# Kernel optimization log

Hardware: AMD Instinct MI355X
Metric: run time of the kernel (lower is better)

Reference implementation:

```python
import jax, jax.numpy as jnp
import numpy as np

B, T, V, C = 64, 256, 256, 4
NEG = -jnp.inf


def setup_inputs() -> dict:
    key = jax.random.key(0)
    k1, k2, k3 = jax.random.split(key, 3)
    logits = jax.random.normal(k1, (B, T, V, C), dtype=jnp.float32)
    ar_sent = jax.random.randint(k2, (B, T), 0, 61, dtype=jnp.int32)
    en_sent = jax.random.randint(k3, (B, V), 0, 61, dtype=jnp.int32)
    return {"logits": logits, "ar_sent": ar_sent, "en_sent": en_sent}


def _forward_alpha(ins, dele, sub):
    # ins/dele/sub: [B,T,V] log-scores of insertion/deletion/substitution into cell (t,v)
    b, t_len, v_len = ins.shape
    z = jnp.zeros((b, 1), ins.dtype)
    # row t=0: only insertions -> prefix sum
    alpha0 = jnp.concatenate([z, jnp.cumsum(ins[:, 0, 1:], axis=1)], axis=1)

    def step(prev, xs):
        ins_t, del_t, sub_t = xs  # each [B,V]
        # c[v]: contributions from previous row (deletion + substitution)
        c = jnp.concatenate(
            [del_t[:, :1] + prev[:, :1],
             jnp.logaddexp(del_t[:, 1:] + prev[:, 1:], sub_t[:, 1:] + prev[:, :-1])],
            axis=1)
        # within-row recurrence alpha[v] = logaddexp(ins[v]+alpha[v-1], c[v])
        # solved in closed form: alpha[v] = S[v] + logcumsumexp_k<=v (c[k]-S[k]), S=prefix sum of ins
        s = jnp.concatenate([z, jnp.cumsum(ins_t[:, 1:], axis=1)], axis=1)
        row = s + jax.lax.cumlogsumexp(c - s, axis=1)
        return row, row

    xs = (jnp.moveaxis(ins, 1, 0)[1:], jnp.moveaxis(dele, 1, 0)[1:], jnp.moveaxis(sub, 1, 0)[1:])
    _, rows = jax.lax.scan(step, alpha0, xs)
    return jnp.moveaxis(jnp.concatenate([alpha0[None], rows], axis=0), 0, 1)  # [B,T,V]


def _backward_beta(ins, dele, sub):
    b, t_len, v_len = ins.shape
    z = jnp.zeros((b, 1), ins.dtype)
    # row t=T-1: only insertions -> suffix sum, corner = 0
    ins_last = ins[:, -1, :]
    beta_last = jnp.concatenate([jnp.cumsum(ins_last[:, -2::-1], axis=1)[:, ::-1], z], axis=1)

    def step(nxt, xs):
        ins_t, del_t, sub_t = xs
        # c[v]: contributions from next row (deletion + substitution); v=V-1 has no substitution
        c = jnp.concatenate(
            [jnp.logaddexp(del_t[:, :-1] + nxt[:, :-1], sub_t[:, :-1] + nxt[:, 1:]),
             del_t[:, -1:] + nxt[:, -1:]],
            axis=1)
        # beta[v] = logaddexp(ins[v]+beta[v+1], c[v]): reverse linear recurrence -> flip + closed form
        fins = ins_t[:, ::-1]
        fc = c[:, ::-1]
        fs = jnp.concatenate([z, jnp.cumsum(fins[:, 1:], axis=1)], axis=1)
        fb = fs + jax.lax.cumlogsumexp(fc - fs, axis=1)
        row = fb[:, ::-1]
        return row, row

    xs = (jnp.moveaxis(ins, 1, 0)[:-1][::-1],
          jnp.moveaxis(dele, 1, 0)[:-1][::-1],
          jnp.moveaxis(sub, 1, 0)[:-1][::-1])
    _, rows = jax.lax.scan(step, beta_last, xs)
    beta = jnp.concatenate([rows[::-1], beta_last[None]], axis=0)
    return jnp.moveaxis(beta, 0, 1)  # [B,T,V]


def reference(logits, ar_sent, en_sent):
    # tiny_table class ids: deletion=0, insertion=1, substitution=2 (constant, char-independent)
    scores = jax.nn.log_softmax(logits, axis=3)  # [B,T,V,4]
    dele, ins, sub = scores[..., 0], scores[..., 1], scores[..., 2]
    alpha = _forward_alpha(ins, dele, sub)

    # beta / expected counts are computed under no_grad in the original
    sg = jax.lax.stop_gradient
    s = sg(scores)
    a = sg(alpha)
    beta = _backward_beta(s[..., 1], s[..., 0], s[..., 2])

    bsz, t_len, v_len, n_cls = scores.shape
    cls = jnp.arange(n_cls)[None, None, :]
    t_lt = (jnp.arange(t_len) < t_len - 1)[:, None, None]
    v_lt = (jnp.arange(v_len) < v_len - 1)[None, :, None]
    pd = jnp.broadcast_to(jnp.where((cls == 0) & t_lt, 0.0, NEG), (t_len, v_len, n_cls))
    pi = jnp.broadcast_to(jnp.where((cls == 1) & v_lt, 0.0, NEG), (t_len, v_len, n_cls))
    ps = jnp.broadcast_to(jnp.where((cls == 2) & t_lt & v_lt, 0.0, NEG), (t_len, v_len, n_cls))

    full = jnp.full((bsz, t_len, v_len, n_cls), NEG, scores.dtype)
    ed = full.at[:, 1:].set(a[:, :-1, :, None] + s[:, 1:] + pd[None, 1:] + beta[:, 1:, :, None])
    ei = full.at[:, :, 1:].set(a[:, :, :-1, None] + s[:, :, 1:] + pi[None, :, 1:] + beta[:, :, 1:, None])
    es = full.at[:, 1:, 1:].set(
        a[:, :-1, :-1, None] + s[:, 1:, 1:] + ps[None, 1:, 1:] + beta[:, 1:, 1:, None])

    ec = jnp.logaddexp(jnp.logaddexp(ed, ei), es)
    norm = jax.nn.logsumexp(ec, axis=3, keepdims=True)
    norm = jnp.where(jnp.isneginf(norm), 0.0, norm)  # avoid nan at degenerate (0,0)-type cells
    expected_counts = jnp.exp(ec - norm)
    return (scores, expected_counts, alpha[0, -1, -1])
```

## Files before the change

kernel.cpp:

```cpp
#include <hip/hip_runtime.h>
#include <math.h>

#define BB 64
#define TT 256
#define VV 256
#define SLABS 321
#define SLAB_F (SLABS * 256)
#define PLANE ((size_t)BB * SLAB_F)
#define EPLANE ((size_t)BB * SLABS * 64)
#define NSLAB_W 319

typedef __attribute__((ext_vector_type(4))) _Float16 half4;

__device__ __forceinline__ float dpp_shr1_f(float x) {
    return __int_as_float(__builtin_amdgcn_update_dpp(
        __float_as_int(x), __float_as_int(x), 0x138, 0xF, 0xF, false));
}
__device__ __forceinline__ int dpp_shr1_i(int x) {
    return __builtin_amdgcn_update_dpp(x, x, 0x138, 0xF, 0xF, false);
}

__device__ __forceinline__ float lae2(float x, float y) {
    float m = fmaxf(x, y);
    float d = x - y;
    return m + __logf(1.0f + __expf(-fabsf(d)));
}

__global__ void __launch_bounds__(256) k_prep(const float4* __restrict__ lg,
                                              float4* __restrict__ sc,
                                              _Float16* __restrict__ Dd,
                                              _Float16* __restrict__ Di,
                                              _Float16* __restrict__ Du) {
    int blk = blockIdx.x;
    int b = blk / NSLAB_W;
    int s = blk - b * NSLAB_W;
    int v = threadIdx.x;
    int t = s - (v >> 2);
    bool valid = (t >= 0) && (t < TT);
    int tc = valid ? t : 0;
    size_t ci = ((size_t)b << 16) | ((size_t)tc << 8) | (size_t)v;
    float4 x = lg[ci];
    float m = fmaxf(fmaxf(x.x, x.y), fmaxf(x.z, x.w));
    float e0 = __expf(x.x - m), e1 = __expf(x.y - m);
    float e2 = __expf(x.z - m), e3 = __expf(x.w - m);
    float ssum = e0 + e1 + e2 + e3;
    float l = m + __logf(ssum);
    if (valid) sc[ci] = make_float4(x.x - l, x.y - l, x.z - l, x.w - l);
    float rcp = valid ? (1.0f / ssum) : 0.0f;
    size_t pb = (size_t)b * SLAB_F + ((size_t)s << 8) + v;
    Dd[pb] = (_Float16)(e0 * rcp);
    Di[pb] = (_Float16)(e1 * rcp);
    Du[pb] = (_Float16)(e2 * rcp);
}

__global__ void __launch_bounds__(128) k_dp(const _Float16* __restrict__ Pd,
                                            const _Float16* __restrict__ Pi,
                                            const _Float16* __restrict__ Pu,
                                            float* __restrict__ A,
                                            int* __restrict__ Ei,
                                            float* __restrict__ scalar_out) {
    const int b = (blockIdx.x << 1) | (threadIdx.x >> 6);
    const int lane = threadIdx.x & 63;
    const bool l0 = (lane == 0);
    const size_t base = (size_t)b * SLAB_F + (lane << 2);

    const half4* __restrict__ pd = (const half4*)(Pd + base);
    const half4* __restrict__ pi = (const half4*)(Pi + base);
    const half4* __restrict__ pu = (const half4*)(Pu + base);
    float4* __restrict__ pa = (float4*)(A + base);
    int* __restrict__ pe = Ei + (size_t)b * SLABS * 64 + lane;
    const int SS = 64;

    half4 d0,d1,d2,d3,d4,d5,d6,d7;
    half4 i0,i1,i2,i3,i4,i5,i6,i7;
    half4 u0,u1,u2,u3,u4,u5,u6,u7;
    d0 = pd[0*SS]; i0 = pi[0*SS]; u0 = pu[0*SS];
    d1 = pd[1*SS]; i1 = pi[1*SS]; u1 = pu[1*SS];
    d2 = pd[2*SS]; i2 = pi[2*SS]; u2 = pu[2*SS];
    d3 = pd[3*SS]; i3 = pi[3*SS]; u3 = pu[3*SS];
    d4 = pd[4*SS]; i4 = pi[4*SS]; u4 = pu[4*SS];
    d5 = pd[5*SS]; i5 = pi[5*SS]; u5 = pu[5*SS];
    d6 = pd[6*SS]; i6 = pi[6*SS]; u6 = pu[6*SS];
    d7 = pd[7*SS]; i7 = pi[7*SS]; u7 = pu[7*SS];

    float A0 = 0.0f, A1 = 0.0f, A2 = 0.0f, A3 = 0.0f;
    int   E  = 0;
    float LC = 0.0f, LP = 0.0f;
    int   EC = 0,    EP = 0;
    float sA3 = 0.0f;
    int   sEn = 0;

    int s = 0;

#define STEP(DD, II, UU, FIXUP, CLAMP, CAP)                                       \
    {                                                                             \
        const half4 dl = DD, in = II, su = UU;                                    \
        {                                                                         \
            int sp = s + 8;                                                       \
            if (CLAMP) sp = sp > SLABS - 1 ? SLABS - 1 : sp;                      \
            DD = pd[sp * SS]; II = pi[sp * SS]; UU = pu[sp * SS];                 \
        }                                                                         \
        int E_eff = E;                                                            \
        bool isT0 = false;                                                        \
        if (FIXUP) {                                                              \
            isT0 = (s == lane);                                                   \
            E_eff = isT0 ? (l0 ? 0 : EC) : E;                                     \
        }                                                                         \
        const float lc = l0 ? 0.0f : ldexpf(LC, EC - E_eff);                      \
        const float lp = l0 ? 0.0f : ldexpf(LP, EP - E_eff);                      \
        float X0 = (float)dl.x * A0 + (float)su.x * lp;                           \
        float X1 = (float)dl.y * A1 + (float)su.y * A0;                           \
        float X2 = (float)dl.z * A2 + (float)su.z * A1;                           \
        float X3 = (float)dl.w * A3 + (float)su.w * A2;                           \
        if (FIXUP && isT0) {                                                      \
            X0 = l0 ? 1.0f : 0.0f; X1 = 0.0f; X2 = 0.0f; X3 = 0.0f;               \
        }                                                                         \
        const float iy = (float)in.y, iz = (float)in.z, iw = (float)in.w;         \
        const float B0 = X0;                                                      \
        const float B1 = fmaf(B0, iy, X1);                                        \
        const float B2 = fmaf(B1, iz, X2);                                        \
        const float B3 = fmaf(B2, iw, X3);                                        \
        const float Q0 = (float)in.x;                                             \
        const float Q1 = Q0 * iy;                                                 \
        const float Q2 = Q1 * iz;                                                 \
        const float Q3 = Q2 * iw;                                                 \
        float nA0 = fmaf(lc, Q0, B0);                                             \
        float nA1 = fmaf(lc, Q1, B1);                                             \
        float nA2 = fmaf(lc, Q2, B2);                                             \
        float nA3 = fmaf(lc, Q3, B3);                                             \
        const int eb = (int)((__float_as_uint(nA3) >> 23) & 255u) - 126;          \
        const int En = E_eff + eb;                                                \
        nA3 = ldexpf(nA3, -eb);                                                   \
        nA0 = ldexpf(nA0, -eb);                                                   \
        nA1 = ldexpf(nA1, -eb);                                                   \
        nA2 = ldexpf(nA2, -eb);                                                   \
        LP = LC; EP = EC;                                                         \
        LC = dpp_shr1_f(nA3);                                                     \
        EC = dpp_shr1_i(En);                                                      \
        pa[s * SS] = make_float4(nA0, nA1, nA2, nA3);                             \
        pe[s * 64] = En;                                                          \
        if (CAP && s == TT + 62) { sA3 = nA3; sEn = En; }     \
        A0 = nA0; A1 = nA1; A2 = nA2; A3 = nA3; E = En;                           \
        ++s;                                                                      \
    }

#pragma unroll 1
    for (int it = 0; it < 8; ++it) {
        STEP(d0, i0, u0, 1, 0, 0);
        STEP(d1, i1, u1, 1, 0, 0);
        STEP(d2, i2, u2, 1, 0, 0);
        STEP(d3, i3, u3, 1, 0, 0);
        STEP(d4, i4, u4, 1, 0, 0);
        STEP(d5, i5, u5, 1, 0, 0);
        STEP(d6, i6, u6, 1, 0, 0);
        STEP(d7, i7, u7, 1, 0, 0);
    }
#pragma unroll 1
    for (int it = 0; it < 31; ++it) {
        STEP(d0, i0, u0, 0, 0, 0);
        STEP(d1, i1, u1, 0, 0, 0);
        STEP(d2, i2, u2, 0, 0, 0);
        STEP(d3, i3, u3, 0, 0, 0);
        STEP(d4, i4, u4, 0, 0, 0);
        STEP(d5, i5, u5, 0, 0, 0);
        STEP(d6, i6, u6, 0, 0, 0);
        STEP(d7, i7, u7, 0, 0, 0);
    }
    STEP(d0, i0, u0, 0, 1, 1);
    STEP(d1, i1, u1, 0, 1, 1);
    STEP(d2, i2, u2, 0, 1, 1);
    STEP(d3, i3, u3, 0, 1, 1);
    STEP(d4, i4, u4, 0, 1, 1);
    STEP(d5, i5, u5, 0, 1, 1);
    STEP(d6, i6, u6, 0, 1, 1);
    STEP(d7, i7, u7, 0, 1, 1);
#undef STEP

    if ((b == 0) && (lane == 63))
        scalar_out[0] = logf(sA3) + (float)sEn * 0.6931471805599453f;
}

__global__ void __launch_bounds__(256) k_counts(const _Float16* __restrict__ Pd,
                                                const _Float16* __restrict__ Pi,
                                                const _Float16* __restrict__ Pu,
                                                const float* __restrict__ A,
                                                const int* __restrict__ Ei,
                                                float4* __restrict__ out) {
    int blk = blockIdx.x;
    int b = blk / NSLAB_W;
    int s = blk - b * NSLAB_W;
    int v = threadIdx.x;
    int g = v >> 2;
    int t = s - g;
    if ((t < 0) | (t >= TT)) return;

    size_t ab = (size_t)b * SLAB_F;
    size_t ebp = (size_t)b * SLABS * 64;
    int sm1 = s > 0 ? s - 1 : 0;
    int sm2 = s > 1 ? s - 2 : 0;
    int vm = v ? v - 1 : 0;
    int gm = g ? g - 1 : 0;
    bool v4 = (v & 3) == 0;

    float pD = (float)Pd[ab + ((size_t)s << 8) + v];
    float pI = (float)Pi[ab + ((size_t)s << 8) + v];
    float pU = (float)Pu[ab + ((size_t)s << 8) + v];
    float AA = A[ab + ((size_t)s   << 8) + v];
    float AU = A[ab + ((size_t)sm1 << 8) + v];
    int   EA = Ei[ebp + s   * 64 + g];
    int   EU = Ei[ebp + sm1 * 64 + g];
    float AL = v4 ? A[ab + ((size_t)sm1 << 8) + vm] : A[ab + ((size_t)s   << 8) + vm];
    int   EL = v4 ? Ei[ebp + sm1 * 64 + gm] : EA;
    float AD = v4 ? A[ab + ((size_t)sm2 << 8) + vm] : A[ab + ((size_t)sm1 << 8) + vm];
    int   ED = v4 ? Ei[ebp + sm2 * 64 + gm] : EU;

    bool tE = (t == 0) | (t == TT - 1);
    bool vE = (v == 0) | (v == VV - 1);
    float inv = 1.0f / AA;
    float w0 = ldexpf(pD * AU * inv, EU - EA);
    float w1 = ldexpf(pI * AL * inv, EL - EA);
    float w2 = ldexpf(pU * AD * inv, ED - EA);
    float4 o;
    o.x = tE ? 0.0f : (vE ? 1.0f : w0);
    o.y = vE ? 0.0f : (tE ? 1.0f : w1);
    o.z = (tE | vE) ? 0.0f : w2;
    o.w = 0.0f;
    out[((size_t)b << 16) | ((size_t)t << 8) | (size_t)v] = o;
}

__global__ void k_prep_legacy(const float4* __restrict__ lg, float4* __restrict__ sc, int n) {
    int i = blockIdx.x * blockDim.x + threadIdx.x;
    int st = gridDim.x * blockDim.x;
    for (; i < n; i += st) {
        float4 x = lg[i];
        float m = fmaxf(fmaxf(x.x, x.y), fmaxf(x.z, x.w));
        float s = __expf(x.x - m) + __expf(x.y - m) + __expf(x.z - m) + __expf(x.w - m);
        float l = m + __logf(s);
        sc[i] = make_float4(x.x - l, x.y - l, x.z - l, x.w - l);
    }
}
__global__ void __launch_bounds__(64) k_dp_legacy(const float4* __restrict__ scores,
                                                  float4* __restrict__ counts,
                                                  float* __restrict__ scalar_out) {
    const int b = blockIdx.x;
    const int lane = threadIdx.x;
    const int v0 = lane << 2;
    const float4* __restrict__ srow = scores + ((size_t)b * TT * VV + v0);
    float4* __restrict__ crow = counts + ((size_t)b * TT * VV + v0);
    float4 P0[4], P1[4], P2[4];
    {
        int r; const float4* p;
        r = 0 - lane; r = r < 0 ? 0 : r; p = srow + (size_t)r * VV;
        P0[0]=p[0]; P0[1]=p[1]; P0[2]=p[2]; P0[3]=p[3];
        r = 1 - lane; r = r < 0 ? 0 : r; p = srow + (size_t)r * VV;
        P1[0]=p[0]; P1[1]=p[1]; P1[2]=p[2]; P1[3]=p[3];
        r = 2 - lane; r = r < 0 ? 0 : r; p = srow + (size_t)r * VV;
        P2[0]=p[0]; P2[1]=p[1]; P2[2]=p[2]; P2[3]=p[3];
    }
    float aPrev[4] = { -INFINITY, -INFINITY, -INFINITY, -INFINITY };
    float leftPrev = -INFINITY, leftCur = -INFINITY;
    int s = 0;
#define STEPL(BUF)                                                                \
    {                                                                             \
        const int t = s - lane;                                                   \
        const bool active = (t >= 0) && (t < TT);                                 \
        float4 c0 = BUF[0], c1 = BUF[1], c2 = BUF[2], c3 = BUF[3];                \
        {                                                                         \
            int tp = t + 3; tp = tp < 0 ? 0 : tp; tp = tp > TT - 1 ? TT - 1 : tp; \
            const float4* lp = srow + (size_t)tp * VV;                            \
            BUF[0]=lp[0]; BUF[1]=lp[1]; BUF[2]=lp[2]; BUF[3]=lp[3];               \
        }                                                                         \
        float aPm1_0 = (lane == 0) ? -INFINITY : leftPrev;                        \
        float cv0 = lae2(c0.x + aPrev[0], c0.z + aPm1_0);                         \
        float cv1 = lae2(c1.x + aPrev[1], c1.z + aPrev[0]);                       \
        float cv2 = lae2(c2.x + aPrev[2], c2.z + aPrev[1]);                       \
        float cv3 = lae2(c3.x + aPrev[3], c3.z + aPrev[2]);                       \
        if (lane == 0) cv0 = c0.x + aPrev[0];                                     \
        if (t == 0) {                                                             \
            cv0 = (lane == 0) ? 0.0f : -INFINITY;                                 \
            cv1 = -INFINITY; cv2 = -INFINITY; cv3 = -INFINITY;                    \
        }                                                                         \
        float lc = (lane == 0) ? -INFINITY : leftCur;                             \
        float a0 = lae2(lc + c0.y, cv0);                                          \
        float a1 = lae2(a0 + c1.y, cv1);                                          \
        float a2 = lae2(a1 + c2.y, cv2);                                          \
        float a3 = lae2(a2 + c3.y, cv3);                                          \
        if (active) {                                                             \
            const bool tE = (t == 0) | (t == TT - 1);                             \
            float aCm1[4] = { lc, a0, a1, a2 };                                   \
            float aPm1[4] = { aPm1_0, aPrev[0], aPrev[1], aPrev[2] };             \
            float aP[4]   = { aPrev[0], aPrev[1], aPrev[2], aPrev[3] };           \
            float aA[4]   = { a0, a1, a2, a3 };                                   \
            float4 sv[4]  = { c0, c1, c2, c3 };                                   \
            float4* cp = crow + (size_t)t * VV;                                   \
            _Pragma("unroll")                                                     \
            for (int k = 0; k < 4; ++k) {                                         \
                const bool vE = (k == 0 && lane == 0) || (k == 3 && lane == 63);  \
                float w0 = __expf(aP[k]   + sv[k].x - aA[k]);                     \
                float w1 = __expf(aCm1[k] + sv[k].y - aA[k]);                     \
                float w2 = __expf(aPm1[k] + sv[k].z - aA[k]);                     \
                float4 o;                                                         \
                o.x = tE ? 0.0f : (vE ? 1.0f : w0);                               \
                o.y = vE ? 0.0f : (tE ? 1.0f : w1);                               \
                o.z = (tE || vE) ? 0.0f : w2;                                     \
                o.w = 0.0f;                                                       \
                cp[k] = o;                                                        \
            }                                                                     \
            if ((t == TT - 1) && (lane == 63) && (b == 0)) scalar_out[0] = a3;    \
        }                                                                         \
        aPrev[0]=a0; aPrev[1]=a1; aPrev[2]=a2; aPrev[3]=a3;                       \
        leftPrev = leftCur;                                                       \
        leftCur = __shfl_up(a3, 1);                                               \
        ++s;                                                                      \
    }
#pragma unroll 1
    for (int it = 0; it < 107; ++it) { STEPL(P0); STEPL(P1); STEPL(P2); }
#undef STEPL
}

extern "C" void kernel_launch(void* const* d_in, const int* in_sizes, int n_in,
                              void* d_out, int out_size, void* d_ws, size_t ws_size,
                              hipStream_t stream) {
    const float* logits = (const float*)d_in[0];
    float* out = (float*)d_out;
    const size_t ncell = (size_t)BB * TT * VV;

    float4* scores = (float4*)out;
    float4* counts = (float4*)(out + ncell * 4);
    float* scalar_out = out + ncell * 8;

    _Float16* Pd = (_Float16*)d_ws;
    _Float16* Pi = Pd + PLANE;
    _Float16* Pu = Pi + PLANE;
    float* Aa = (float*)(Pu + PLANE);
    int*   Ee = (int*)(Aa + PLANE);

    size_t need = PLANE * 2 * 3 + PLANE * 4 + EPLANE * 4;
    if (ws_size >= need) {
        k_prep<<<BB * NSLAB_W, 256, 0, stream>>>((const float4*)logits, scores, Pd, Pi, Pu);
        k_dp<<<BB / 2, 128, 0, stream>>>(Pd, Pi, Pu, Aa, Ee, scalar_out);
        k_counts<<<BB * NSLAB_W, 256, 0, stream>>>(Pd, Pi, Pu, Aa, Ee, counts);
    } else {
        k_prep_legacy<<<2048, 256, 0, stream>>>((const float4*)logits, scores, (int)ncell);
        k_dp_legacy<<<BB, 64, 0, stream>>>(scores, counts, scalar_out);
    }
}
```

Before: 112.4 us.

## Fuse DP scan and counts into one kernel with progress-flag overlap

Merges the serial DP kernel and the counts kernel into a single launch. 32 blocks run the wavefront recurrence and publish per-batch progress through release atomics every 32 slabs. The remaining persistent blocks spin on those flags and compute expected counts for completed slabs, so the counts pass overlaps the latency-bound DP instead of running after it. This adds a memset, spin-wait polling and fences, and it relies on the DP blocks being scheduled alongside the consumer blocks to avoid deadlock.

```diff
diff --git a/kernel.cpp b/kernel.cpp
--- a/kernel.cpp
+++ b/kernel.cpp
@@ -9,6 +9,7 @@
 #define PLANE ((size_t)BB * SLAB_F)
 #define EPLANE ((size_t)BB * SLABS * 64)
 #define NSLAB_W 319
+#define NCNT 704
 
 typedef __attribute__((ext_vector_type(4))) _Float16 half4;
 
@@ -53,44 +54,47 @@
     Du[pb] = (_Float16)(e2 * rcp);
 }
 
-__global__ void __launch_bounds__(128) k_dp(const _Float16* __restrict__ Pd,
-                                            const _Float16* __restrict__ Pi,
-                                            const _Float16* __restrict__ Pu,
-                                            float* __restrict__ A,
-                                            int* __restrict__ Ei,
-                                            float* __restrict__ scalar_out) {
-    const int b = (blockIdx.x << 1) | (threadIdx.x >> 6);
-    const int lane = threadIdx.x & 63;
-    const bool l0 = (lane == 0);
-    const size_t base = (size_t)b * SLAB_F + (lane << 2);
-
-    const half4* __restrict__ pd = (const half4*)(Pd + base);
-    const half4* __restrict__ pi = (const half4*)(Pi + base);
-    const half4* __restrict__ pu = (const half4*)(Pu + base);
-    float4* __restrict__ pa = (float4*)(A + base);
-    int* __restrict__ pe = Ei + (size_t)b * SLABS * 64 + lane;
-    const int SS = 64;
-
-    half4 d0,d1,d2,d3,d4,d5,d6,d7;
-    half4 i0,i1,i2,i3,i4,i5,i6,i7;
-    half4 u0,u1,u2,u3,u4,u5,u6,u7;
-    d0 = pd[0*SS]; i0 = pi[0*SS]; u0 = pu[0*SS];
-    d1 = pd[1*SS]; i1 = pi[1*SS]; u1 = pu[1*SS];
-    d2 = pd[2*SS]; i2 = pi[2*SS]; u2 = pu[2*SS];
-    d3 = pd[3*SS]; i3 = pi[3*SS]; u3 = pu[3*SS];
-    d4 = pd[4*SS]; i4 = pi[4*SS]; u4 = pu[4*SS];
-    d5 = pd[5*SS]; i5 = pi[5*SS]; u5 = pu[5*SS];
-    d6 = pd[6*SS]; i6 = pi[6*SS]; u6 = pu[6*SS];
-    d7 = pd[7*SS]; i7 = pi[7*SS]; u7 = pu[7*SS];
-
-    float A0 = 0.0f, A1 = 0.0f, A2 = 0.0f, A3 = 0.0f;
-    int   E  = 0;
-    float LC = 0.0f, LP = 0.0f;
-    int   EC = 0,    EP = 0;
-    float sA3 = 0.0f;
-    int   sEn = 0;
-
-    int s = 0;
+__global__ void __launch_bounds__(256) k_dpcnt(const _Float16* __restrict__ Pd,
+                                               const _Float16* __restrict__ Pi,
+                                               const _Float16* __restrict__ Pu,
+                                               float* __restrict__ A,
+                                               int* __restrict__ Ei,
+                                               float* __restrict__ scalar_out,
+                                               int* __restrict__ progress,
+                                               float4* __restrict__ out) {
+    if (blockIdx.x < 32) {
+        if (threadIdx.x >= 128) return;
+        const int b = (blockIdx.x << 1) | (threadIdx.x >> 6);
+        const int lane = threadIdx.x & 63;
+        const bool l0 = (lane == 0);
+        const size_t base = (size_t)b * SLAB_F + (lane << 2);
+
+        const half4* __restrict__ pd = (const half4*)(Pd + base);
+        const half4* __restrict__ pi = (const half4*)(Pi + base);
+        const half4* __restrict__ pu = (const half4*)(Pu + base);
+        float4* __restrict__ pa = (float4*)(A + base);
+        int* __restrict__ pe = Ei + (size_t)b * SLABS * 64 + lane;
+        const int SS = 64;
+
+        half4 d0,d1,d2,d3,d4,d5,d6,d7;
+        half4 i0,i1,i2,i3,i4,i5,i6,i7;
+        half4 u0,u1,u2,u3,u4,u5,u6,u7;
+        d0 = pd[0*SS]; i0 = pi[0*SS]; u0 = pu[0*SS];
+        d1 = pd[1*SS]; i1 = pi[1*SS]; u1 = pu[1*SS];
+        d2 = pd[2*SS]; i2 = pi[2*SS]; u2 = pu[2*SS];
+        d3 = pd[3*SS]; i3 = pi[3*SS]; u3 = pu[3*SS];
+        d4 = pd[4*SS]; i4 = pi[4*SS]; u4 = pu[4*SS];
+        d5 = pd[5*SS]; i5 = pi[5*SS]; u5 = pu[5*SS];
+        d6 = pd[6*SS]; i6 = pi[6*SS]; u6 = pu[6*SS];
+        d7 = pd[7*SS]; i7 = pi[7*SS]; u7 = pu[7*SS];
+
+        float A0 = 0.0f, A1 = 0.0f, A2 = 0.0f, A3 = 0.0f;
+        int   E  = 0;
+        float LC = 0.0f, LP = 0.0f;
+        int   EC = 0,    EP = 0;
+        float sA3 = 0.0f;
+        int   sEn = 0;
+        int s = 0;
 
 #define STEP(DD, II, UU, FIXUP, CLAMP, CAP)                                       \
     {                                                                             \
@@ -139,93 +143,112 @@
         EC = dpp_shr1_i(En);                                                      \
         pa[s * SS] = make_float4(nA0, nA1, nA2, nA3);                             \
         pe[s * 64] = En;                                                          \
-        if (CAP && s == TT + 62) { sA3 = nA3; sEn = En; }     \
+        if (CAP && s == TT + 62) { sA3 = nA3; sEn = En; }                         \
         A0 = nA0; A1 = nA1; A2 = nA2; A3 = nA3; E = En;                           \
         ++s;                                                                      \
     }
+#define PUBLISH()                                                                 \
+    {                                                                             \
+        __threadfence();                                                          \
+        if (l0) __hip_atomic_store(&progress[b], s - 1, __ATOMIC_RELEASE,         \
+                                   __HIP_MEMORY_SCOPE_AGENT);                     \
+    }
 
 #pragma unroll 1
-    for (int it = 0; it < 8; ++it) {
-        STEP(d0, i0, u0, 1, 0, 0);
-        STEP(d1, i1, u1, 1, 0, 0);
-        STEP(d2, i2, u2, 1, 0, 0);
-        STEP(d3, i3, u3, 1, 0, 0);
-        STEP(d4, i4, u4, 1, 0, 0);
-        STEP(d5, i5, u5, 1, 0, 0);
-        STEP(d6, i6, u6, 1, 0, 0);
-        STEP(d7, i7, u7, 1, 0, 0);
-    }
+        for (int it = 0; it < 8; ++it) {
+            STEP(d0, i0, u0, 1, 0, 0);
+            STEP(d1, i1, u1, 1, 0, 0);
+            STEP(d2, i2, u2, 1, 0, 0);
+            STEP(d3, i3, u3, 1, 0, 0);
+            STEP(d4, i4, u4, 1, 0, 0);
+            STEP(d5, i5, u5, 1, 0, 0);
+            STEP(d6, i6, u6, 1, 0, 0);
+            STEP(d7, i7, u7, 1, 0, 0);
+            if ((it & 3) == 3) PUBLISH();
+        }
 #pragma unroll 1
-    for (int it = 0; it < 31; ++it) {
-        STEP(d0, i0, u0, 0, 0, 0);
-        STEP(d1, i1, u1, 0, 0, 0);
-        STEP(d2, i2, u2, 0, 0, 0);
-        STEP(d3, i3, u3, 0, 0, 0);
-        STEP(d4, i4, u4, 0, 0, 0);
-        STEP(d5, i5, u5, 0, 0, 0);
-        STEP(d6, i6, u6, 0, 0, 0);
-        STEP(d7, i7, u7, 0, 0, 0);
-    }
-    STEP(d0, i0, u0, 0, 1, 1);
-    STEP(d1, i1, u1, 0, 1, 1);
-    STEP(d2, i2, u2, 0, 1, 1);
-    STEP(d3, i3, u3, 0, 1, 1);
-    STEP(d4, i4, u4, 0, 1, 1);
-    STEP(d5, i5, u5, 0, 1, 1);
-    STEP(d6, i6, u6, 0, 1, 1);
-    STEP(d7, i7, u7, 0, 1, 1);
+        for (int it = 0; it < 31; ++it) {
+            STEP(d0, i0, u0, 0, 0, 0);
+            STEP(d1, i1, u1, 0, 0, 0);
+            STEP(d2, i2, u2, 0, 0, 0);
+            STEP(d3, i3, u3, 0, 0, 0);
+            STEP(d4, i4, u4, 0, 0, 0);
+            STEP(d5, i5, u5, 0, 0, 0);
+            STEP(d6, i6, u6, 0, 0, 0);
+            STEP(d7, i7, u7, 0, 0, 0);
+            if ((it & 3) == 3) PUBLISH();
+        }
+        STEP(d0, i0, u0, 0, 1, 1);
+        STEP(d1, i1, u1, 0, 1, 1);
+        STEP(d2, i2, u2, 0, 1, 1);
+        STEP(d3, i3, u3, 0, 1, 1);
+        STEP(d4, i4, u4, 0, 1, 1);
+        STEP(d5, i5, u5, 0, 1, 1);
+        STEP(d6, i6, u6, 0, 1, 1);
+        STEP(d7, i7, u7, 0, 1, 1);
+        PUBLISH();
 #undef STEP
-
-    if ((b == 0) && (lane == 63))
-        scalar_out[0] = logf(sA3) + (float)sEn * 0.6931471805599453f;
-}
-
-__global__ void __launch_bounds__(256) k_counts(const _Float16* __restrict__ Pd,
-                                                const _Float16* __restrict__ Pi,
-                                                const _Float16* __restrict__ Pu,
-                                                const float* __restrict__ A,
-                                                const int* __restrict__ Ei,
-                                                float4* __restrict__ out) {
-    int blk = blockIdx.x;
-    int b = blk / NSLAB_W;
-    int s = blk - b * NSLAB_W;
-    int v = threadIdx.x;
-    int g = v >> 2;
-    int t = s - g;
-    if ((t < 0) | (t >= TT)) return;
-
-    size_t ab = (size_t)b * SLAB_F;
-    size_t ebp = (size_t)b * SLABS * 64;
-    int sm1 = s > 0 ? s - 1 : 0;
-    int sm2 = s > 1 ? s - 2 : 0;
-    int vm = v ? v - 1 : 0;
-    int gm = g ? g - 1 : 0;
-    bool v4 = (v & 3) == 0;
-
-    float pD = (float)Pd[ab + ((size_t)s << 8) + v];
-    float pI = (float)Pi[ab + ((size_t)s << 8) + v];
-    float pU = (float)Pu[ab + ((size_t)s << 8) + v];
-    float AA = A[ab + ((size_t)s   << 8) + v];
-    float AU = A[ab + ((size_t)sm1 << 8) + v];
-    int   EA = Ei[ebp + s   * 64 + g];
-    int   EU = Ei[ebp + sm1 * 64 + g];
-    float AL = v4 ? A[ab + ((size_t)sm1 << 8) + vm] : A[ab + ((size_t)s   << 8) + vm];
-    int   EL = v4 ? Ei[ebp + sm1 * 64 + gm] : EA;
-    float AD = v4 ? A[ab + ((size_t)sm2 << 8) + vm] : A[ab + ((size_t)sm1 << 8) + vm];
-    int   ED = v4 ? Ei[ebp + sm2 * 64 + gm] : EU;
-
-    bool tE = (t == 0) | (t == TT - 1);
-    bool vE = (v == 0) | (v == VV - 1);
-    float inv = 1.0f / AA;
-    float w0 = ldexpf(pD * AU * inv, EU - EA);
-    float w1 = ldexpf(pI * AL * inv, EL - EA);
-    float w2 = ldexpf(pU * AD * inv, ED - EA);
-    float4 o;
-    o.x = tE ? 0.0f : (vE ? 1.0f : w0);
-    o.y = vE ? 0.0f : (tE ? 1.0f : w1);
-    o.z = (tE | vE) ? 0.0f : w2;
-    o.w = 0.0f;
-    out[((size_t)b << 16) | ((size_t)t << 8) | (size_t)v] = o;
+#undef PUBLISH
+
+        if ((b == 0) && (lane == 63))
+            scalar_out[0] = logf(sA3) + (float)sEn * 0.6931471805599453f;
+    } else {
+        const int G = (int)gridDim.x - 32;
+        const int v = threadIdx.x;
+        const int g = v >> 2;
+        __shared__ int s_go;
+        for (int task = (int)blockIdx.x - 32; task < 64 * NSLAB_W; task += G) {
+            int s = task >> 6;
+            int b = task & 63;
+            if (v == 0) {
+                while (__hip_atomic_load(&progress[b], __ATOMIC_ACQUIRE,
+                                         __HIP_MEMORY_SCOPE_AGENT) < s)
+                    __builtin_amdgcn_s_sleep(2);
+                s_go = 1;
+            }
+            __syncthreads();
+            (void)s_go;
+
+            int t = s - g;
+            bool act = (t >= 0) && (t < TT);
+            if (act) {
+                size_t ab = (size_t)b * SLAB_F;
+                size_t ebp = (size_t)b * SLABS * 64;
+                int sm1 = s > 0 ? s - 1 : 0;
+                int sm2 = s > 1 ? s - 2 : 0;
+                int vm = v ? v - 1 : 0;
+                int gm = g ? g - 1 : 0;
+                bool v4 = (v & 3) == 0;
+
+                float pD = (float)Pd[ab + ((size_t)s << 8) + v];
+                float pI = (float)Pi[ab + ((size_t)s << 8) + v];
+                float pU = (float)Pu[ab + ((size_t)s << 8) + v];
+                float AA = A[ab + ((size_t)s   << 8) + v];
+                float AU = A[ab + ((size_t)sm1 << 8) + v];
+                int   EA = Ei[ebp + s   * 64 + g];
+                int   EU = Ei[ebp + sm1 * 64 + g];
+                float AL = v4 ? A[ab + ((size_t)sm1 << 8) + vm]
+                              : A[ab + ((size_t)s   << 8) + vm];
+                int   EL = v4 ? Ei[ebp + sm1 * 64 + gm] : EA;
+                float AD = v4 ? A[ab + ((size_t)sm2 << 8) + vm]
+                              : A[ab + ((size_t)sm1 << 8) + vm];
+                int   ED = v4 ? Ei[ebp + sm2 * 64 + gm] : EU;
+
+                bool tE = (t == 0) | (t == TT - 1);
+                bool vE = (v == 0) | (v == VV - 1);
+                float inv = 1.0f / AA;
+                float w0 = ldexpf(pD * AU * inv, EU - EA);
+                float w1 = ldexpf(pI * AL * inv, EL - EA);
+                float w2 = ldexpf(pU * AD * inv, ED - EA);
+                float4 o;
+                o.x = tE ? 0.0f : (vE ? 1.0f : w0);
+                o.y = vE ? 0.0f : (tE ? 1.0f : w1);
+                o.z = (tE | vE) ? 0.0f : w2;
+                o.w = 0.0f;
+                out[((size_t)b << 16) | ((size_t)t << 8) | (size_t)v] = o;
+            }
+        }
+    }
 }
 
 __global__ void k_prep_legacy(const float4* __restrict__ lg, float4* __restrict__ sc, int n) {
@@ -334,12 +357,13 @@
     _Float16* Pu = Pi + PLANE;
     float* Aa = (float*)(Pu + PLANE);
     int*   Ee = (int*)(Aa + PLANE);
-
-    size_t need = PLANE * 2 * 3 + PLANE * 4 + EPLANE * 4;
+    int*   prog = Ee + EPLANE;
+
+    size_t need = PLANE * 2 * 3 + PLANE * 4 + EPLANE * 4 + 64 * 4;
     if (ws_size >= need) {
         k_prep<<<BB * NSLAB_W, 256, 0, stream>>>((const float4*)logits, scores, Pd, Pi, Pu);
-        k_dp<<<BB / 2, 128, 0, stream>>>(Pd, Pi, Pu, Aa, Ee, scalar_out);
-        k_counts<<<BB * NSLAB_W, 256, 0, stream>>>(Pd, Pi, Pu, Aa, Ee, counts);
+        hipMemsetAsync(prog, 0xFF, 64 * sizeof(int), stream);
+        k_dpcnt<<<32 + NCNT, 256, 0, stream>>>(Pd, Pi, Pu, Aa, Ee, scalar_out, prog, counts);
     } else {
         k_prep_legacy<<<2048, 256, 0, stream>>>((const float4*)logits, scores, (int)ncell);
         k_dp_legacy<<<BB, 64, 0, stream>>>(scores, counts, scalar_out);
```

Result: slower. 377.9 us (+236.3%).
